# Optimization experiments

Measured on AMD Instinct MI355X. Metric: run time of the kernel, lower is better.

The kernel has to match this reference:

```python
import jax, jax.numpy as jnp
import numpy as np

DIM = 128
HOP = 2
NEIGH = [12, 2]  # neighbor_num per hop
ALPHA = 0.2      # leaky-relu slope
NUM_NODE = 50000
B, S = 128, 50
STDV = 1.0 / np.sqrt(DIM)


def _leaky(x):
    return jnp.where(x >= 0, x, ALPHA * x)


def _local_agg(h, adj, a_local):
    # h: [B,S,D], adj: [B,S,S] ints in 0..4, a_local: [4,D]
    a_in = h[:, :, None, :] * h[:, None, :, :]            # [B,S,S,D]
    e = _leaky(jnp.einsum('bijd,kd->kbij', a_in, a_local))  # [4,B,S,S]
    att = jnp.full(adj.shape, -9e15, dtype=h.dtype)
    for k in range(4):
        att = jnp.where(adj == k + 1, e[k], att)
    att = jax.nn.softmax(att, axis=-1)
    return jnp.einsum('bij,bjd->bid', att, h)


def _global_agg(self_v, neigh_v, extra_v, w1, w2, w3, bias):
    # self_v: [B,N,D], neigh_v: [B,N,K,D], extra_v: [B,N,D]
    a = _leaky(jnp.einsum('bnkd,de->bnke', extra_v[:, :, None, :] * neigh_v, w1))
    a = jnp.einsum('bnke,e->bnk', a, w2)
    a = jax.nn.softmax(a, axis=-1)
    agg = jnp.einsum('bnk,bnkd->bnd', a, neigh_v)
    out = jnp.concatenate([self_v, agg], axis=-1) @ w3 + bias
    return jax.nn.relu(out)


def setup_inputs() -> dict:
    key = jax.random.key(0)
    ks = jax.random.split(key, 12)
    u = lambda k, shp: jax.random.uniform(k, shp, jnp.float32, -STDV, STDV)
    return {
        'inputs': jax.random.randint(ks[0], (B, S), 0, NUM_NODE),
        'adj': jax.random.randint(ks[1], (B, S, S), 0, 5),
        'mask_item': jnp.ones((B, S), dtype=jnp.int32),
        'item': jax.random.randint(ks[2], (B, S), 0, NUM_NODE),
        'first_adj': jax.random.randint(ks[3], (B, S * NEIGH[0]), 0, NUM_NODE),
        'adj_all': jax.random.randint(ks[4], (NUM_NODE, 2), 0, NUM_NODE),
        'embedding': u(ks[5], (NUM_NODE, DIM)),
        'a_local': u(ks[6], (4, DIM)),
        'gw1': u(ks[7], (HOP, DIM, DIM)),
        'gw2': u(ks[8], (HOP, DIM)),
        'gw3': u(ks[9], (HOP, 2 * DIM, DIM)),
        'gbias': u(ks[10], (HOP, DIM)),
    }


def reference(inputs, adj, mask_item, item, first_adj, adj_all,
              embedding, a_local, gw1, gw2, gw3, gbias):
    b, s = inputs.shape
    h = embedding[inputs]                                  # [B,S,D]
    h_local = _local_agg(h, adj, a_local)

    m = mask_item.astype(embedding.dtype)[..., None]       # [B,S,1]
    item_emb = embedding[item] * m
    sum_item = jnp.sum(item_emb, 1) / jnp.sum(m, 1)        # [B,D]
    sess = sum_item[:, None, :]                            # [B,1,D]

    # multi-hop neighbor sampling
    neigh1 = first_adj.reshape(b, s * NEIGH[0])            # [B, 600]
    neigh2 = adj_all[neigh1.reshape(-1)].reshape(b, s * NEIGH[0] * NEIGH[1])  # [B,1200]
    ev = [embedding[inputs], embedding[neigh1], embedding[neigh2]]

    for n_hop in range(HOP):
        nxt = []
        for hop in range(HOP - n_hop):
            neigh_v = ev[hop + 1].reshape(b, -1, NEIGH[hop], DIM)
            extra_v = jnp.broadcast_to(sess, (b, ev[hop].shape[1], DIM))
            nxt.append(_global_agg(ev[hop], neigh_v, extra_v,
                                   gw1[n_hop], gw2[n_hop], gw3[n_hop], gbias[n_hop]))
        ev = nxt
    h_global = ev[0].reshape(b, s, DIM)

    # dropout is identity at eval
    return h_local + h_global
```

## Files before the change

### kernel.cpp

```cpp
#include <hip/hip_runtime.h>
#include <stdint.h>

typedef unsigned short ushort_t;
typedef __attribute__((ext_vector_type(8))) short bf16x8;
typedef __attribute__((ext_vector_type(4))) float f32x4;

#define B_   128
#define S_   50
#define D_   128
#define ALPHA_ 0.2f

__device__ __forceinline__ float bf2f(ushort_t u){
  return __uint_as_float(((uint32_t)u) << 16);
}
__device__ __forceinline__ ushort_t f2bf(float f){
  uint32_t x = __float_as_uint(f);
  x = (x + 0x7fffu + ((x >> 16) & 1u)) >> 16;
  return (ushort_t)x;
}
__device__ __forceinline__ float leaky(float x){ return x >= 0.f ? x : ALPHA_*x; }

__device__ __forceinline__ int detect_flag_block(const uint32_t* __restrict__ emb_raw){
  __shared__ int flg;
  if (threadIdx.x == 0){
    int ok = 1;
    for (int i = 0; i < 64; i++){
      uint32_t lo = emb_raw[i] & 0xffffu;
      uint32_t ex = (lo >> 7) & 0xFFu;
      if (!(lo == 0u || (ex >= 64u && ex <= 126u))) ok = 0;
    }
    flg = ok;
  }
  __syncthreads();
  return flg;
}

#define NLOCAL_ 512
#define NSESS_  64
#define NCVT_   3174
#define NPREP_  48
#define CVT_BASE_   (NLOCAL_ + NSESS_)
#define PREP_BASE_  (CVT_BASE_ + NCVT_)
#define K1_GRID_    (PREP_BASE_ + NPREP_)

__global__ __launch_bounds__(256) void k1(
    const int* __restrict__ inputs, const int* __restrict__ adj,
    const int* __restrict__ item, const int* __restrict__ mask,
    const void* __restrict__ p0, const void* __restrict__ p1,
    const void* __restrict__ p2, const void* __restrict__ p3,
    const void* __restrict__ p4, const void* __restrict__ p5,
    ushort_t* __restrict__ emb_b, uint4* __restrict__ w1f, uint4* __restrict__ w3f,
    ushort_t* __restrict__ sessb, ushort_t* __restrict__ hlb)
{
  int blk = blockIdx.x, tid = threadIdx.x;
  int flag = detect_flag_block((const uint32_t*)p0);

  if (blk < NLOCAL_){
    __shared__ ushort_t hS[64][136];
    __shared__ float    attS[16][68];
    __shared__ int      sids[64];
    __shared__ ushort_t alS[512];
    int b  = blk >> 2;
    int mi = blk & 3;
    if (tid < 64) sids[tid] = (tid < S_) ? inputs[b*S_ + tid] : 0;
    for (int i = tid; i < 512; i += 256)
      alS[i] = flag ? ((const ushort_t*)p1)[i] : f2bf(((const float*)p1)[i]);
    __syncthreads();
    if (flag){
      const ushort_t* e16 = (const ushort_t*)p0;
      for (int idx = tid; idx < 64*16; idx += 256){
        int j = idx >> 4, ch = idx & 15;
        uint4 v = {0u, 0u, 0u, 0u};
        if (j < S_) v = *(const uint4*)(e16 + (size_t)sids[j]*D_ + ch*8);
        *(uint4*)(&hS[j][ch*8]) = v;
      }
    } else {
      const float* ef = (const float*)p0;
      for (int idx = tid; idx < 64*32; idx += 256){
        int j = idx >> 5, ch = idx & 31;
        union { ushort_t u[4]; uint2 d2; } o;
        o.d2 = make_uint2(0u, 0u);
        if (j < S_){
          float4 v = *(const float4*)(ef + (size_t)sids[j]*D_ + ch*4);
          o.u[0]=f2bf(v.x); o.u[1]=f2bf(v.y); o.u[2]=f2bf(v.z); o.u[3]=f2bf(v.w);
        }
        *(uint2*)(&hS[j][ch*4]) = o.d2;
      }
    }
    for (int idx = tid; idx < 16*64; idx += 256)
      attS[idx >> 6][idx & 63] = -9.0e15f;
    __syncthreads();

    int lane = tid & 63, wv = tid >> 6;
    int q = lane >> 4, c = lane & 15;

    f32x4 Eacc[4];
    #pragma unroll
    for (int ni = 0; ni < 4; ni++) Eacc[ni] = (f32x4){0.f,0.f,0.f,0.f};
    #pragma unroll
    for (int kt = 0; kt < 4; kt++){
      uint4 av = *(const uint4*)(alS + wv*D_ + kt*32 + q*8);
      const uint32_t* ap = (const uint32_t*)&av;
      uint4 hv = *(const uint4*)(&hS[mi*16 + c][kt*32 + q*8]);
      const uint32_t* hp = (const uint32_t*)&hv;
      union { ushort_t u[8]; bf16x8 v; } afr;
      #pragma unroll
      for (int p = 0; p < 4; p++){
        float x0 = __uint_as_float(hp[p] << 16)         * __uint_as_float(ap[p] << 16);
        float x1 = __uint_as_float(hp[p] & 0xffff0000u) * __uint_as_float(ap[p] & 0xffff0000u);
        afr.u[2*p]   = f2bf(x0);
        afr.u[2*p+1] = f2bf(x1);
      }
      #pragma unroll
      for (int ni = 0; ni < 4; ni++){
        union { uint4 q4; bf16x8 v; } bfr;
        bfr.q4 = *(const uint4*)(&hS[ni*16 + c][kt*32 + q*8]);
        Eacc[ni] = __builtin_amdgcn_mfma_f32_16x16x32_bf16(afr.v, bfr.v, Eacc[ni], 0,0,0);
      }
    }
    const int* adjb = adj + (size_t)b*S_*S_;
    #pragma unroll
    for (int ni = 0; ni < 4; ni++){
      int j = ni*16 + c;
      #pragma unroll
      for (int r = 0; r < 4; r++){
        int i = mi*16 + q*4 + r;
        if (i < S_ && j < S_){
          int kk = adjb[i*S_ + j];
          if (kk == wv + 1) attS[q*4 + r][j] = leaky(Eacc[ni][r]);
        }
      }
    }
    __syncthreads();
    {
      int r  = tid >> 4;
      int cg = tid & 15;
      int i  = mi*16 + r;
      float v0 = attS[r][cg*4+0], v1 = attS[r][cg*4+1];
      float v2 = attS[r][cg*4+2], v3 = attS[r][cg*4+3];
      float mx = fmaxf(fmaxf(v0,v1), fmaxf(v2,v3));
      #pragma unroll
      for (int off = 1; off < 16; off <<= 1) mx = fmaxf(mx, __shfl_xor(mx, off, 16));
      float e0 = (cg*4+0 < S_) ? __expf(v0 - mx) : 0.f;
      float e1 = (cg*4+1 < S_) ? __expf(v1 - mx) : 0.f;
      float e2 = (cg*4+2 < S_) ? __expf(v2 - mx) : 0.f;
      float e3 = (cg*4+3 < S_) ? __expf(v3 - mx) : 0.f;
      float s = e0 + e1 + e2 + e3;
      #pragma unroll
      for (int off = 1; off < 16; off <<= 1) s += __shfl_xor(s, off, 16);
      float inv = (i < S_) ? 1.f / s : 0.f;
      attS[r][cg*4+0] = e0*inv;
      attS[r][cg*4+1] = e1*inv;
      attS[r][cg*4+2] = e2*inv;
      attS[r][cg*4+3] = e3*inv;
    }
    __syncthreads();
    f32x4 Pacc[2];
    Pacc[0] = (f32x4){0.f,0.f,0.f,0.f};
    Pacc[1] = (f32x4){0.f,0.f,0.f,0.f};
    #pragma unroll
    for (int kt = 0; kt < 2; kt++){
      union { ushort_t u[8]; bf16x8 v; } afr;
      const float* arow = &attS[c][kt*32 + q*8];
      #pragma unroll
      for (int j = 0; j < 8; j++) afr.u[j] = f2bf(arow[j]);
      #pragma unroll
      for (int nn = 0; nn < 2; nn++){
        int ni = 2*wv + nn;
        union { ushort_t u[8]; bf16x8 v; } bfr;
        #pragma unroll
        for (int jj = 0; jj < 8; jj++)
          bfr.u[jj] = hS[kt*32 + q*8 + jj][ni*16 + c];
        Pacc[nn] = __builtin_amdgcn_mfma_f32_16x16x32_bf16(afr.v, bfr.v, Pacc[nn], 0,0,0);
      }
    }
    #pragma unroll
    for (int nn = 0; nn < 2; nn++){
      int d = (2*wv + nn)*16 + c;
      #pragma unroll
      for (int r = 0; r < 4; r++){
        int i = mi*16 + q*4 + r;
        if (i < S_) hlb[((size_t)b*S_ + i)*D_ + d] = f2bf(Pacc[nn][r]);
      }
    }
  } else if (blk < CVT_BASE_){
    int b = (blk - NLOCAL_)*2 + (tid >> 7);
    int d = tid & 127;
    float acc = 0.f, den = 0.f;
    if (flag){
      const ushort_t* e16 = (const ushort_t*)p0;
      for (int s = 0; s < S_; s++){
        float fm = (float)mask[b*S_ + s];
        int id = item[b*S_ + s];
        acc += fm * bf2f(e16[(size_t)id*D_ + d]);
        den += fm;
      }
    } else {
      const float* ef = (const float*)p0;
      for (int s = 0; s < S_; s++){
        float fm = (float)mask[b*S_ + s];
        int id = item[b*S_ + s];
        acc += fm * ef[(size_t)id*D_ + d];
        den += fm;
      }
    }
    sessb[b*D_ + d] = f2bf(acc / den);
  } else if (blk < PREP_BASE_){
    const int seg_end[6] = {6400000, 6400512, 6433280, 6433536, 6499072, 6499328};
    int base = ((blk - CVT_BASE_)*256 + tid) * 8;
    if (base >= 6499328) return;
    int s = 0;
    while (base >= seg_end[s]) s++;
    int segbase = (s == 0) ? 0 : seg_end[s-1];
    const void* src = (s==0)?p0:(s==1)?p1:(s==2)?p2:(s==3)?p3:(s==4)?p4:p5;
    int off = base - segbase;
    union { ushort_t u[8]; uint4 q4; } o;
    if (flag){
      o.q4 = *(const uint4*)((const ushort_t*)src + off);
    } else {
      const float* fp = (const float*)src + off;
      float4 v0 = *(const float4*)(fp);
      float4 v1 = *(const float4*)(fp + 4);
      o.u[0]=f2bf(v0.x); o.u[1]=f2bf(v0.y); o.u[2]=f2bf(v0.z); o.u[3]=f2bf(v0.w);
      o.u[4]=f2bf(v1.x); o.u[5]=f2bf(v1.y); o.u[6]=f2bf(v1.z); o.u[7]=f2bf(v1.w);
    }
    *(uint4*)(emb_b + base) = o.q4;
  } else {
    int id = (blk - PREP_BASE_)*256 + tid;
    if (id >= 12288) return;
    if (id < 4096){
      int h = id >> 11, i = id & 2047;
      int kt = i >> 9, rem = i & 511, t = rem >> 6, ln = rem & 63;
      int q = ln >> 4, c = ln & 15;
      union { ushort_t u[8]; uint4 q4; } e;
      #pragma unroll
      for (int j = 0; j < 8; j++){
        int idx = h*16384 + (32*kt + q*8 + j)*128 + 16*t + c;
        e.u[j] = flag ? ((const ushort_t*)p2)[idx] : f2bf(((const float*)p2)[idx]);
      }
      w1f[h*2048 + i] = e.q4;
    } else {
      int id2 = id - 4096;
      int h = id2 >> 12, i = id2 & 4095;
      int kt = i >> 9, rem = i & 511, t = rem >> 6, ln = rem & 63;
      int q = ln >> 4, c = ln & 15;
      union { ushort_t u[8]; uint4 q4; } e;
      #pragma unroll
      for (int j = 0; j < 8; j++){
        int idx = h*32768 + (32*kt + q*8 + j)*128 + 16*t + c;
        e.u[j] = flag ? ((const ushort_t*)p4)[idx] : f2bf(((const float*)p4)[idx]);
      }
      w3f[h*4096 + i] = e.q4;
    }
  }
}

#define NT2TPREP_ 1564
#define NT2SCORE_ 768
#define K2_GRID_  (NT2TPREP_ + NT2SCORE_)

__global__ __launch_bounds__(256) void k2(
    const ushort_t* __restrict__ emb, const uint4* __restrict__ w3f,
    ushort_t* __restrict__ Tt, ushort_t* __restrict__ Tb,
    const ushort_t* __restrict__ sessb,
    const int* __restrict__ neigh1, const int* __restrict__ adj_all,
    const uint4* __restrict__ w1f, const ushort_t* __restrict__ w2,
    float* __restrict__ score)
{
  __shared__ uint4 frag[2048];
  __shared__ ushort_t sS[128];
  int blk = blockIdx.x, tid = threadIdx.x;

  if (blk < NT2TPREP_){
    int half = blk & 1;
    int rowbase = (blk >> 1) * 64;
    for (int i = tid; i < 2048; i += 256) frag[i] = w3f[half*2048 + i];
    __syncthreads();
    int lane = tid & 63, wave = tid >> 6;
    int m = lane & 15, q = lane >> 4;
    int row = rowbase + wave*16 + m;
    int rowc = row < 50000 ? row : 49999;
    f32x4 acc[8];
    #pragma unroll
    for (int t = 0; t < 8; t++) acc[t] = (f32x4){0.f,0.f,0.f,0.f};
    #pragma unroll
    for (int kt = 0; kt < 4; kt++){
      union { uint4 q4; bf16x8 v; } bfr;
      bfr.q4 = *(const uint4*)(emb + (size_t)rowc*D_ + kt*32 + q*8);
      #pragma unroll
      for (int t = 0; t < 8; t++){
        union { uint4 q4; bf16x8 v; } af;
        af.q4 = frag[(kt*8 + t)*64 + lane];
        acc[t] = __builtin_amdgcn_mfma_f32_16x16x32_bf16(af.v, bfr.v, acc[t], 0, 0, 0);
      }
    }
    if (row < 50000){
      ushort_t* dst = (half ? Tb : Tt) + (size_t)row*D_;
      #pragma unroll
      for (int t = 0; t < 8; t++){
        int col0 = 16*t + q*4;
        union { ushort_t u[4]; uint2 d2; } pk;
        #pragma unroll
        for (int r = 0; r < 4; r++) pk.u[r] = f2bf(acc[t][r]);
        *(uint2*)(dst + col0) = pk.d2;
      }
    }
    return;
  }

  int b2  = blk - NT2TPREP_;
  int sb  = b2 / 6;
  int sub = b2 - sb*6;
  int grp = sub >> 1;
  int halft = sub & 1;
  if (tid < 16) ((uint4*)sS)[tid] = ((const uint4*)(sessb + (size_t)sb*D_))[tid];
  __syncthreads();
  for (int i = tid; i < 2048; i += 256){
    int kt = i >> 9, ln = i & 63, q = (ln >> 4);
    uint4 w = w1f[i];
    uint4 sv = *(const uint4*)(sS + kt*32 + q*8);
    const ushort_t* wu = (const ushort_t*)&w;
    const ushort_t* su = (const ushort_t*)&sv;
    union { ushort_t u[8]; uint4 q4; } o;
    #pragma unroll
    for (int j = 0; j < 8; j++) o.u[j] = f2bf(bf2f(wu[j]) * bf2f(su[j]));
    frag[i] = o.q4;
  }
  __syncthreads();
  int lane = tid & 63, wave = tid >> 6;
  int m = lane & 15, q = lane >> 4;
  float w2v[8];
  #pragma unroll
  for (int t = 0; t < 8; t++) w2v[t] = bf2f(w2[16*t + m]);

  int tend = halft ? 38 : 19;
  for (int t = halft*19 + wave; t < tend; t += 4){
    int rr = t*16 + m;
    int rrc = rr < 599 ? rr : 599;
    int nid;
    if (grp == 0){
      nid = neigh1[sb*600 + rrc];
    } else {
      int r2 = sb*1200 + (grp-1)*600 + rrc;
      nid = adj_all[(size_t)neigh1[r2 >> 1]*2 + (r2 & 1)];
    }
    const ushort_t* nrow = emb + (size_t)nid*D_;
    f32x4 acc[8];
    #pragma unroll
    for (int t8 = 0; t8 < 8; t8++) acc[t8] = (f32x4){0.f,0.f,0.f,0.f};
    #pragma unroll
    for (int kt = 0; kt < 4; kt++){
      union { uint4 q4; bf16x8 v; } af;
      af.q4 = *(const uint4*)(nrow + kt*32 + q*8);
      #pragma unroll
      for (int t8 = 0; t8 < 8; t8++){
        union { uint4 q4; bf16x8 v; } bf;
        bf.q4 = frag[(kt*8 + t8)*64 + lane];
        acc[t8] = __builtin_amdgcn_mfma_f32_16x16x32_bf16(af.v, bf.v, acc[t8], 0, 0, 0);
      }
    }
    #pragma unroll
    for (int r = 0; r < 4; r++){
      float s = 0.f;
      #pragma unroll
      for (int t8 = 0; t8 < 8; t8++) s += leaky(acc[t8][r]) * w2v[t8];
      s += __shfl_xor(s, 1, 64);
      s += __shfl_xor(s, 2, 64);
      s += __shfl_xor(s, 4, 64);
      s += __shfl_xor(s, 8, 64);
      if (m == 0){
        int rw = t*16 + q*4 + r;
        if (rw < 600){
          int sidx = (grp == 0) ? (sb*600 + rw)
                                : (76800 + sb*1200 + (grp-1)*600 + rw);
          score[sidx] = s;
        }
      }
    }
  }
}

__global__ __launch_bounds__(256) void score2_c(
    const ushort_t* __restrict__ sessb, const ushort_t* __restrict__ out1,
    const uint4* __restrict__ w1f, const ushort_t* __restrict__ w2,
    float* __restrict__ score)
{
  __shared__ uint4 bfrag[2048];
  __shared__ ushort_t sS[128];
  int blk = blockIdx.x, tid = threadIdx.x;
  int sb  = blk >> 2;
  int qtr = blk & 3;
  if (tid < 16) ((uint4*)sS)[tid] = ((const uint4*)(sessb + (size_t)sb*D_))[tid];
  __syncthreads();
  for (int i = tid; i < 2048; i += 256){
    int kt = i >> 9, ln = i & 63, q = (ln >> 4);
    uint4 w = w1f[i];
    uint4 sv = *(const uint4*)(sS + kt*32 + q*8);
    const ushort_t* wu = (const ushort_t*)&w;
    const ushort_t* su = (const ushort_t*)&sv;
    union { ushort_t u[8]; uint4 q4; } o;
    #pragma unroll
    for (int j = 0; j < 8; j++) o.u[j] = f2bf(bf2f(wu[j]) * bf2f(su[j]));
    bfrag[i] = o.q4;
  }
  __syncthreads();
  int lane = tid & 63, wave = tid >> 6;
  int m = lane & 15, q = lane >> 4;
  float w2v[8];
  #pragma unroll
  for (int t = 0; t < 8; t++) w2v[t] = bf2f(w2[16*t + m]);

  int t0 = qtr*10, tend = (qtr*10 + 10 < 38) ? qtr*10 + 10 : 38;
  for (int t = t0 + wave; t < tend; t += 4){
    int rr = t*16 + m;
    int rrc = rr < 599 ? rr : 599;
    const ushort_t* nrow = out1 + ((size_t)sb*600 + rrc)*D_;
    f32x4 acc[8];
    #pragma unroll
    for (int t8 = 0; t8 < 8; t8++) acc[t8] = (f32x4){0.f,0.f,0.f,0.f};
    #pragma unroll
    for (int kt = 0; kt < 4; kt++){
      union { uint4 q4; bf16x8 v; } af;
      af.q4 = *(const uint4*)(nrow + kt*32 + q*8);
      #pragma unroll
      for (int t8 = 0; t8 < 8; t8++){
        union { uint4 q4; bf16x8 v; } bf;
        bf.q4 = bfrag[(kt*8 + t8)*64 + lane];
        acc[t8] = __builtin_amdgcn_mfma_f32_16x16x32_bf16(af.v, bf.v, acc[t8], 0, 0, 0);
      }
    }
    #pragma unroll
    for (int r = 0; r < 4; r++){
      float s = 0.f;
      #pragma unroll
      for (int t8 = 0; t8 < 8; t8++) s += leaky(acc[t8][r]) * w2v[t8];
      s += __shfl_xor(s, 1, 64);
      s += __shfl_xor(s, 2, 64);
      s += __shfl_xor(s, 4, 64);
      s += __shfl_xor(s, 8, 64);
      if (m == 0){
        int rw = t*16 + q*4 + r;
        if (rw < 600) score[sb*600 + rw] = s;
      }
    }
  }
}

template<int K>
__device__ __forceinline__ void softmaxK(const float* __restrict__ sc, float att[K]){
  float mx = -__builtin_inff();
  #pragma unroll
  for (int k = 0; k < K; k++){ att[k] = sc[k]; mx = fmaxf(mx, att[k]); }
  float s = 0.f;
  #pragma unroll
  for (int k = 0; k < K; k++){ att[k] = __expf(att[k] - mx); s += att[k]; }
  float inv = 1.f / s;
  #pragma unroll
  for (int k = 0; k < K; k++) att[k] *= inv;
}

template<int K>
__device__ __forceinline__ void out_tile(
    int lane, const uint4* __restrict__ afrag,
    const ushort_t* __restrict__ sptr, const ushort_t* const nptr[K],
    const float att[K], f32x4 acc[8]){
  int q = lane >> 4;
  #pragma unroll
  for (int kt = 0; kt < 8; kt++){
    union { ushort_t u[8]; uint4 q4; bf16x8 v; } bfr;
    if (kt < 4){
      bfr.q4 = *(const uint4*)(sptr + kt*32 + q*8);
    } else {
      float g[8] = {0,0,0,0,0,0,0,0};
      #pragma unroll
      for (int k = 0; k < K; k++){
        uint4 nv = *(const uint4*)(nptr[k] + (kt-4)*32 + q*8);
        const uint32_t* np = (const uint32_t*)&nv;
        #pragma unroll
        for (int p = 0; p < 4; p++){
          g[2*p]   = fmaf(att[k], __uint_as_float(np[p] << 16),         g[2*p]);
          g[2*p+1] = fmaf(att[k], __uint_as_float(np[p] & 0xffff0000u), g[2*p+1]);
        }
      }
      #pragma unroll
      for (int j = 0; j < 8; j++) bfr.u[j] = f2bf(g[j]);
    }
    #pragma unroll
    for (int t = 0; t < 8; t++){
      union { uint4 q4; bf16x8 v; } af;
      af.q4 = afrag[(kt*8 + t)*64 + lane];
      acc[t] = __builtin_amdgcn_mfma_f32_16x16x32_bf16(af.v, bfr.v, acc[t], 0, 0, 0);
    }
  }
}

__global__ __launch_bounds__(256) void gather_out(
    const int* __restrict__ idx, const int* __restrict__ nbr,
    const int* __restrict__ adj_all, const float* __restrict__ score,
    const ushort_t* __restrict__ Tt, const ushort_t* __restrict__ Tb,
    const ushort_t* __restrict__ bias,
    ushort_t* __restrict__ o0c, ushort_t* __restrict__ out1c,
    int nA50, int nTot, int scoreBbase)
{
  int row  = (blockIdx.x*256 + threadIdx.x) >> 6;
  int lane = threadIdx.x & 63;
  if (row >= nTot) return;
  row = __builtin_amdgcn_readfirstlane(row);
  float b0 = bf2f(bias[lane*2]), b1 = bf2f(bias[lane*2 + 1]);
  float acc0, acc1;
  ushort_t* dst;
  if (row < nA50){
    float att[12];
    softmaxK<12>(score + (size_t)row*12, att);
    uint32_t sv = *(const uint32_t*)(Tt + (size_t)idx[row]*D_ + lane*2);
    acc0 = __uint_as_float(sv << 16);
    acc1 = __uint_as_float(sv & 0xffff0000u);
    #pragma unroll
    for (int k = 0; k < 12; k++){
      uint32_t nv = *(const uint32_t*)(Tb + (size_t)nbr[row*12 + k]*D_ + lane*2);
      acc0 = fmaf(att[k], __uint_as_float(nv << 16),          acc0);
      acc1 = fmaf(att[k], __uint_as_float(nv & 0xffff0000u),  acc1);
    }
    dst = o0c + (size_t)row*D_;
  } else {
    int rB = row - nA50;
    float att[2];
    softmaxK<2>(score + scoreBbase + (size_t)rB*2, att);
    int self = nbr[rB];
    uint32_t sv = *(const uint32_t*)(Tt + (size_t)self*D_ + lane*2);
    acc0 = __uint_as_float(sv << 16);
    acc1 = __uint_as_float(sv & 0xffff0000u);
    #pragma unroll
    for (int k = 0; k < 2; k++){
      uint32_t nv = *(const uint32_t*)(Tb + (size_t)adj_all[(size_t)self*2 + k]*D_ + lane*2);
      acc0 = fmaf(att[k], __uint_as_float(nv << 16),          acc0);
      acc1 = fmaf(att[k], __uint_as_float(nv & 0xffff0000u),  acc1);
    }
    dst = out1c + (size_t)rB*D_;
  }
  union { ushort_t u[2]; uint32_t d; } pk;
  pk.u[0] = f2bf(fmaxf(acc0 + b0, 0.f));
  pk.u[1] = f2bf(fmaxf(acc1 + b1, 0.f));
  *(uint32_t*)(dst + lane*2) = pk.d;
}

__global__ __launch_bounds__(256) void out_mfma_c2(
    const float* __restrict__ score, const ushort_t* __restrict__ out1,
    const ushort_t* __restrict__ selfsrc, const uint4* __restrict__ w3f,
    const ushort_t* __restrict__ bias,
    const ushort_t* __restrict__ addsrc, float* __restrict__ outf, int nrows){
  __shared__ uint4 afrag[4096];
  int tid = threadIdx.x;
  for (int i = tid; i < 4096; i += 256) afrag[i] = w3f[i];
  __syncthreads();
  int lane = tid & 63, wave = tid >> 6;
  int mrow = lane & 15, q = lane >> 4;
  float bv[8][4];
  #pragma unroll
  for (int t = 0; t < 8; t++){
    const ushort_t* bp = bias + 16*t + q*4;
    #pragma unroll
    for (int r = 0; r < 4; r++) bv[t][r] = bf2f(bp[r]);
  }
  int row_base = blockIdx.x*64 + wave*16;
  int row = row_base + mrow;
  bool active = row < nrows;
  int rowc = active ? row : (nrows - 1);
  const ushort_t* sptr = selfsrc + (size_t)rowc*D_;
  const ushort_t* nptr[12];
  #pragma unroll
  for (int k = 0; k < 12; k++) nptr[k] = out1 + (size_t)(rowc*12 + k)*D_;
  float att[12];
  softmaxK<12>(score + (size_t)rowc*12, att);
  f32x4 acc[8];
  #pragma unroll
  for (int t = 0; t < 8; t++) acc[t] = (f32x4){0.f,0.f,0.f,0.f};
  out_tile<12>(lane, afrag, sptr, nptr, att, acc);
  if (active){
    #pragma unroll
    for (int t = 0; t < 8; t++){
      int col0 = 16*t + q*4;
      float v[4];
      const ushort_t* ap = addsrc + (size_t)row*D_ + col0;
      #pragma unroll
      for (int r = 0; r < 4; r++)
        v[r] = fmaxf(acc[t][r] + bv[t][r], 0.f) + bf2f(ap[r]);
      *(f32x4*)(outf + (size_t)row*D_ + col0) = (f32x4){v[0], v[1], v[2], v[3]};
    }
  }
}

__global__ __launch_bounds__(256) void score_mfma_ab(
    const ushort_t* __restrict__ sessb, const ushort_t* __restrict__ emb,
    const int* __restrict__ neigh1, const int* __restrict__ adj_all,
    const uint4* __restrict__ w1f, const ushort_t* __restrict__ w2,
    float* __restrict__ score, int nA){
  __shared__ uint4 bfrag[2048];
  int tid = threadIdx.x;
  for (int i = tid; i < 2048; i += 256) bfrag[i] = w1f[i];
  __syncthreads();
  int lane = tid & 63, wave = tid >> 6;
  int m = lane & 15, q = lane >> 4;
  float w2v[8];
  #pragma unroll
  for (int t = 0; t < 8; t++) w2v[t] = bf2f(w2[16*t + m]);

  for (int it = 0; it < 2; it++){
    int row_base = blockIdx.x*128 + it*64 + wave*16;
    int row = row_base + m;
    const ushort_t* nrow; int b;
    if (row < nA){
      nrow = emb + (size_t)neigh1[row]*D_;
      b = row / 600;
    } else {
      int r2 = row - nA;
      nrow = emb + (size_t)adj_all[(size_t)neigh1[r2>>1]*2 + (r2&1)]*D_;
      b = r2 / 1200;
    }
    const ushort_t* srow = sessb + (size_t)b*D_;

    f32x4 acc[8];
    #pragma unroll
    for (int t = 0; t < 8; t++) acc[t] = (f32x4){0.f,0.f,0.f,0.f};
    #pragma unroll
    for (int kt = 0; kt < 4; kt++){
      uint4 nv = *(const uint4*)(nrow + kt*32 + q*8);
      uint4 sv = *(const uint4*)(srow + kt*32 + q*8);
      const uint32_t* np = (const uint32_t*)&nv;
      const uint32_t* sp = (const uint32_t*)&sv;
      union { ushort_t u[8]; bf16x8 v; } afr;
      #pragma unroll
      for (int p = 0; p < 4; p++){
        uint32_t n2 = np[p], s2 = sp[p];
        float a0 = __uint_as_float(n2 << 16)          * __uint_as_float(s2 << 16);
        float a1 = __uint_as_float(n2 & 0xffff0000u)  * __uint_as_float(s2 & 0xffff0000u);
        afr.u[2*p]   = f2bf(a0);
        afr.u[2*p+1] = f2bf(a1);
      }
      #pragma unroll
      for (int t = 0; t < 8; t++){
        union { uint4 q4; bf16x8 v; } bfr;
        bfr.q4 = bfrag[(kt*8 + t)*64 + lane];
        acc[t] = __builtin_amdgcn_mfma_f32_16x16x32_bf16(afr.v, bfr.v, acc[t], 0, 0, 0);
      }
    }
    #pragma unroll
    for (int r = 0; r < 4; r++){
      float s = 0.f;
      #pragma unroll
      for (int t = 0; t < 8; t++) s += leaky(acc[t][r]) * w2v[t];
      s += __shfl_xor(s, 1, 64);
      s += __shfl_xor(s, 2, 64);
      s += __shfl_xor(s, 4, 64);
      s += __shfl_xor(s, 8, 64);
      if (m == 0) score[row_base + q*4 + r] = s;
    }
  }
}

__global__ __launch_bounds__(256) void score_mfma_c(
    const ushort_t* __restrict__ sessb, const ushort_t* __restrict__ out1,
    const uint4* __restrict__ w1f, const ushort_t* __restrict__ w2,
    float* __restrict__ score){
  __shared__ uint4 bfrag[2048];
  int tid = threadIdx.x;
  for (int i = tid; i < 2048; i += 256) bfrag[i] = w1f[i];
  __syncthreads();
  int lane = tid & 63, wave = tid >> 6;
  int m = lane & 15, q = lane >> 4;
  float w2v[8];
  #pragma unroll
  for (int t = 0; t < 8; t++) w2v[t] = bf2f(w2[16*t + m]);
  for (int it = 0; it < 2; it++){
    int row_base = blockIdx.x*128 + it*64 + wave*16;
    int row = row_base + m;
    const ushort_t* nrow = out1 + (size_t)row*D_;
    int b = row / 600;
    const ushort_t* srow = sessb + (size_t)b*D_;
    f32x4 acc[8];
    #pragma unroll
    for (int t = 0; t < 8; t++) acc[t] = (f32x4){0.f,0.f,0.f,0.f};
    #pragma unroll
    for (int kt = 0; kt < 4; kt++){
      uint4 nv = *(const uint4*)(nrow + kt*32 + q*8);
      uint4 sv = *(const uint4*)(srow + kt*32 + q*8);
      const uint32_t* np = (const uint32_t*)&nv;
      const uint32_t* sp = (const uint32_t*)&sv;
      union { ushort_t u[8]; bf16x8 v; } afr;
      #pragma unroll
      for (int p = 0; p < 4; p++){
        uint32_t n2 = np[p], s2 = sp[p];
        float a0 = __uint_as_float(n2 << 16)          * __uint_as_float(s2 << 16);
        float a1 = __uint_as_float(n2 & 0xffff0000u)  * __uint_as_float(s2 & 0xffff0000u);
        afr.u[2*p]   = f2bf(a0);
        afr.u[2*p+1] = f2bf(a1);
      }
      #pragma unroll
      for (int t = 0; t < 8; t++){
        union { uint4 q4; bf16x8 v; } bfr;
        bfr.q4 = bfrag[(kt*8 + t)*64 + lane];
        acc[t] = __builtin_amdgcn_mfma_f32_16x16x32_bf16(afr.v, bfr.v, acc[t], 0, 0, 0);
      }
    }
    #pragma unroll
    for (int r = 0; r < 4; r++){
      float s = 0.f;
      #pragma unroll
      for (int t = 0; t < 8; t++) s += leaky(acc[t][r]) * w2v[t];
      s += __shfl_xor(s, 1, 64);
      s += __shfl_xor(s, 2, 64);
      s += __shfl_xor(s, 4, 64);
      s += __shfl_xor(s, 8, 64);
      if (m == 0) score[row_base + q*4 + r] = s;
    }
  }
}

__global__ __launch_bounds__(512) void out_mfma_ab(
    const float* __restrict__ score, const int* __restrict__ idx,
    const int* __restrict__ nbr, const int* __restrict__ adj_all,
    const ushort_t* __restrict__ emb, const uint4* __restrict__ w3f,
    const ushort_t* __restrict__ bias,
    ushort_t* __restrict__ o0c, ushort_t* __restrict__ out1c,
    int nA, int nTot, int scoreBbase){
  __shared__ uint4 afrag[4096];
  int tid = threadIdx.x;
  for (int i = tid; i < 4096; i += 512) afrag[i] = w3f[i];
  __syncthreads();
  int lane = tid & 63, wave = tid >> 6;
  int mrow = lane & 15, q = lane >> 4;
  float bv[8][4];
  #pragma unroll
  for (int t = 0; t < 8; t++){
    const ushort_t* bp = bias + 16*t + q*4;
    #pragma unroll
    for (int r = 0; r < 4; r++) bv[t][r] = bf2f(bp[r]);
  }
  int row_base = blockIdx.x*128 + wave*16;
  int row = row_base + mrow;
  bool active = row < nTot;
  int rowc = active ? row : (nTot - 1);
  bool isA = rowc < nA;
  f32x4 acc[8];
  #pragma unroll
  for (int t = 0; t < 8; t++) acc[t] = (f32x4){0.f,0.f,0.f,0.f};
  if (isA){
    const ushort_t* sptr = emb + (size_t)idx[rowc]*D_;
    const ushort_t* nptr[12];
    #pragma unroll
    for (int k = 0; k < 12; k++) nptr[k] = emb + (size_t)nbr[rowc*12 + k]*D_;
    float att[12];
    softmaxK<12>(score + (size_t)rowc*12, att);
    out_tile<12>(lane, afrag, sptr, nptr, att, acc);
  } else {
    int rB = rowc - nA;
    const ushort_t* sptr = emb + (size_t)nbr[rB]*D_;
    const ushort_t* nptr[2];
    #pragma unroll
    for (int k = 0; k < 2; k++) nptr[k] = emb + (size_t)adj_all[(size_t)nbr[rB]*2 + k]*D_;
    float att[2];
    softmaxK<2>(score + scoreBbase + (size_t)rB*2, att);
    out_tile<2>(lane, afrag, sptr, nptr, att, acc);
  }
  if (active){
    ushort_t* dst = isA ? (o0c + (size_t)row*D_) : (out1c + (size_t)(row - nA)*D_);
    #pragma unroll
    for (int t = 0; t < 8; t++){
      int col0 = 16*t + q*4;
      union { ushort_t u[4]; uint2 d2; } pk;
      #pragma unroll
      for (int r = 0; r < 4; r++) pk.u[r] = f2bf(fmaxf(acc[t][r] + bv[t][r], 0.f));
      *(uint2*)(dst + col0) = pk.d2;
    }
  }
}

__global__ __launch_bounds__(512) void out_mfma_c(
    const float* __restrict__ score, const ushort_t* __restrict__ out1,
    const ushort_t* __restrict__ selfsrc, const uint4* __restrict__ w3f,
    const ushort_t* __restrict__ bias,
    const ushort_t* __restrict__ addsrc, float* __restrict__ outf, int nrows){
  __shared__ uint4 afrag[4096];
  int tid = threadIdx.x;
  for (int i = tid; i < 4096; i += 512) afrag[i] = w3f[i];
  __syncthreads();
  int lane = tid & 63, wave = tid >> 6;
  int mrow = lane & 15, q = lane >> 4;
  float bv[8][4];
  #pragma unroll
  for (int t = 0; t < 8; t++){
    const ushort_t* bp = bias + 16*t + q*4;
    #pragma unroll
    for (int r = 0; r < 4; r++) bv[t][r] = bf2f(bp[r]);
  }
  int row_base = blockIdx.x*128 + wave*16;
  int row = row_base + mrow;
  bool active = row < nrows;
  int rowc = active ? row : (nrows - 1);
  const ushort_t* sptr = selfsrc + (size_t)rowc*D_;
  const ushort_t* nptr[12];
  #pragma unroll
  for (int k = 0; k < 12; k++) nptr[k] = out1 + (size_t)(rowc*12 + k)*D_;
  float att[12];
  softmaxK<12>(score + (size_t)rowc*12, att);
  f32x4 acc[8];
  #pragma unroll
  for (int t = 0; t < 8; t++) acc[t] = (f32x4){0.f,0.f,0.f,0.f};
  out_tile<12>(lane, afrag, sptr, nptr, att, acc);
  if (active){
    #pragma unroll
    for (int t = 0; t < 8; t++){
      int col0 = 16*t + q*4;
      float v[4];
      const ushort_t* ap = addsrc + (size_t)row*D_ + col0;
      #pragma unroll
      for (int r = 0; r < 4; r++)
        v[r] = fmaxf(acc[t][r] + bv[t][r], 0.f) + bf2f(ap[r]);
      *(f32x4*)(outf + (size_t)row*D_ + col0) = (f32x4){v[0], v[1], v[2], v[3]};
    }
  }
}

extern "C" void kernel_launch(void* const* d_in, const int* in_sizes, int n_in,
                              void* d_out, int out_size, void* d_ws, size_t ws_size,
                              hipStream_t stream) {
  const int* inputs    = (const int*)d_in[0];
  const int* adj       = (const int*)d_in[1];
  const int* mask_item = (const int*)d_in[2];
  const int* item      = (const int*)d_in[3];
  const int* first_adj = (const int*)d_in[4];
  const int* adj_all   = (const int*)d_in[5];

  char* ws = (char*)d_ws;
  size_t o = 0;
  ushort_t* emb_b  = (ushort_t*)(ws + o); o += 12800000;
  ushort_t* alocb  = (ushort_t*)(ws + o); o += 1024;
  ushort_t* gw1b   = (ushort_t*)(ws + o); o += 65536;
  ushort_t* gw2b   = (ushort_t*)(ws + o); o += 512;
  ushort_t* gw3b   = (ushort_t*)(ws + o); o += 131072;
  ushort_t* gbb    = (ushort_t*)(ws + o); o += 512;
  ushort_t* sessb  = (ushort_t*)(ws + o); o += 32768;
  ushort_t* hlb    = (ushort_t*)(ws + o); o += 1638400;
  uint4*    w1f    = (uint4*)(ws + o);    o += 65536;
  uint4*    w3f    = (uint4*)(ws + o);    o += 131072;
  size_t fixed = o;
  (void)alocb; (void)gw1b; (void)gw3b;

  float* outp = (float*)d_out;

  const size_t TPATH_NEED = fixed + 2*(size_t)12800000
                          + (size_t)128*153600
                          + (size_t)128*12800
                          + (size_t)3*128*600*4;
  bool tpath = (ws_size >= TPATH_NEED);

  k1<<<K1_GRID_, 256, 0, stream>>>(
      inputs, adj, item, mask_item,
      d_in[6], d_in[7], d_in[8], d_in[9], d_in[10], d_in[11],
      emb_b, w1f, w3f, sessb, hlb);

  if (tpath){
    ushort_t* Tt    = (ushort_t*)(ws + o);  o += 12800000;
    ushort_t* Tb    = (ushort_t*)(ws + o);  o += 12800000;
    ushort_t* out1c = (ushort_t*)(ws + o);  o += (size_t)128*153600;
    ushort_t* o0c   = (ushort_t*)(ws + o);  o += (size_t)128*12800;
    float*    score = (float*)(ws + o);
    int nA600 = 128*600, nA50 = 128*50, nTot = 128*650;

    k2<<<K2_GRID_, 256, 0, stream>>>(emb_b, w3f, Tt, Tb,
                                     sessb, first_adj, adj_all,
                                     w1f, gw2b, score);
    gather_out<<<(nTot*64 + 255)/256, 256, 0, stream>>>(inputs, first_adj, adj_all, score,
                                                        Tt, Tb, gbb, o0c, out1c,
                                                        nA50, nTot, nA600);
    score2_c<<<512, 256, 0, stream>>>(sessb, out1c, w1f + 2048, gw2b + 128, score);
    out_mfma_c2<<<(nA50 + 63)/64, 256, 0, stream>>>(score, out1c, o0c,
                                                    w3f + 4096, gbb + 128,
                                                    hlb, outp, nA50);
  } else {
    int CHB = 16;
    if      (ws_size >= fixed + (size_t)128*173600) CHB = 128;
    else if (ws_size >= fixed + (size_t)64 *173600) CHB = 64;
    else if (ws_size >= fixed + (size_t)32 *173600) CHB = 32;
    ushort_t* out1c = (ushort_t*)(ws + o);  o += (size_t)CHB*153600;
    ushort_t* o0c   = (ushort_t*)(ws + o);  o += (size_t)CHB*12800;
    float*    score = (float*)(ws + o);

    int nchunk = B_ / CHB;
    for (int c = 0; c < nchunk; c++){
      int b0 = c * CHB;
      const int* fadj  = first_adj + (size_t)b0 * 600;
      const ushort_t* sbc = sessb + (size_t)b0 * D_;
      ushort_t*  hlc   = hlb  + (size_t)b0 * 50 * D_;
      float*     outc  = outp + (size_t)b0 * 50 * D_;
      int nA600 = CHB*600, nA50 = CHB*50, nTot = CHB*650;

      score_mfma_ab<<<(3*nA600)/128, 256, 0, stream>>>(sbc, emb_b, fadj, adj_all,
                                                       w1f, gw2b, score, nA600);
      out_mfma_ab<<<(nTot + 127)/128, 512, 0, stream>>>(score, inputs + b0*50, fadj, adj_all,
                                                        emb_b, w3f, gbb, o0c, out1c,
                                                        nA50, nTot, nA600);
      score_mfma_c<<<nA600/128, 256, 0, stream>>>(sbc, out1c, w1f + 2048, gw2b + 128, score);
      out_mfma_c<<<(nA50 + 127)/128, 512, 0, stream>>>(score, out1c, o0c,
                                                       w3f + 4096, gbb + 128,
                                                       hlc, outc, nA50);
    }
  }
}
```

Before: 195.4 us.

## Skip bf16 embedding copy when input is bf16; reorder and coarsen T-prep blocks

When the embedding table is already bf16 and the T-precompute path is used, k1 no longer copies the whole table into a workspace buffer, and k2 reads the original input directly. The T-prep blocks in k2 now each handle four 64-row tiles, which cuts the grid from 1564 to 392 prep blocks and reuses the weight fragments loaded into shared memory. Those blocks are also placed after the score blocks in the grid. The aim is to remove a 12.8 MB copy and repeated shared-memory fragment loads. In exchange, each prep block does more serial work, and any later kernel that still reads emb_b would see stale data when the input is bf16.

```diff
diff --git a/kernel.cpp b/kernel.cpp
--- a/kernel.cpp
+++ b/kernel.cpp
@@ -50,7 +50,7 @@
     const void* __restrict__ p2, const void* __restrict__ p3,
     const void* __restrict__ p4, const void* __restrict__ p5,
     ushort_t* __restrict__ emb_b, uint4* __restrict__ w1f, uint4* __restrict__ w3f,
-    ushort_t* __restrict__ sessb, ushort_t* __restrict__ hlb)
+    ushort_t* __restrict__ sessb, ushort_t* __restrict__ hlb, int skip_emb)
 {
   int blk = blockIdx.x, tid = threadIdx.x;
   int flag = detect_flag_block((const uint32_t*)p0);
@@ -209,6 +209,7 @@
     const int seg_end[6] = {6400000, 6400512, 6433280, 6433536, 6499072, 6499328};
     int base = ((blk - CVT_BASE_)*256 + tid) * 8;
     if (base >= 6499328) return;
+    if (flag && skip_emb && base < 6400000) return;
     int s = 0;
     while (base >= seg_end[s]) s++;
     int segbase = (s == 0) ? 0 : seg_end[s-1];
@@ -255,12 +256,13 @@
   }
 }
 
-#define NT2TPREP_ 1564
 #define NT2SCORE_ 768
-#define K2_GRID_  (NT2TPREP_ + NT2SCORE_)
+#define NT2TPREP_ 392
+#define K2_GRID_  (NT2SCORE_ + NT2TPREP_)
 
 __global__ __launch_bounds__(256) void k2(
-    const ushort_t* __restrict__ emb, const uint4* __restrict__ w3f,
+    const void* __restrict__ p0, const ushort_t* __restrict__ emb_b,
+    const uint4* __restrict__ w3f,
     ushort_t* __restrict__ Tt, ushort_t* __restrict__ Tb,
     const ushort_t* __restrict__ sessb,
     const int* __restrict__ neigh1, const int* __restrict__ adj_all,
@@ -270,45 +272,52 @@
   __shared__ uint4 frag[2048];
   __shared__ ushort_t sS[128];
   int blk = blockIdx.x, tid = threadIdx.x;
-
-  if (blk < NT2TPREP_){
-    int half = blk & 1;
-    int rowbase = (blk >> 1) * 64;
+  int flag = detect_flag_block((const uint32_t*)p0);
+  const ushort_t* emb = flag ? (const ushort_t*)p0 : emb_b;
+
+  if (blk >= NT2SCORE_){
+    int tp   = blk - NT2SCORE_;
+    int half = tp & 1;
+    int rowbase0 = (tp >> 1) * 256;
     for (int i = tid; i < 2048; i += 256) frag[i] = w3f[half*2048 + i];
     __syncthreads();
     int lane = tid & 63, wave = tid >> 6;
     int m = lane & 15, q = lane >> 4;
-    int row = rowbase + wave*16 + m;
-    int rowc = row < 50000 ? row : 49999;
-    f32x4 acc[8];
-    #pragma unroll
-    for (int t = 0; t < 8; t++) acc[t] = (f32x4){0.f,0.f,0.f,0.f};
-    #pragma unroll
-    for (int kt = 0; kt < 4; kt++){
-      union { uint4 q4; bf16x8 v; } bfr;
-      bfr.q4 = *(const uint4*)(emb + (size_t)rowc*D_ + kt*32 + q*8);
-      #pragma unroll
-      for (int t = 0; t < 8; t++){
-        union { uint4 q4; bf16x8 v; } af;
-        af.q4 = frag[(kt*8 + t)*64 + lane];
-        acc[t] = __builtin_amdgcn_mfma_f32_16x16x32_bf16(af.v, bfr.v, acc[t], 0, 0, 0);
-      }
-    }
-    if (row < 50000){
-      ushort_t* dst = (half ? Tb : Tt) + (size_t)row*D_;
-      #pragma unroll
-      for (int t = 0; t < 8; t++){
-        int col0 = 16*t + q*4;
-        union { ushort_t u[4]; uint2 d2; } pk;
+    ushort_t* Tdst = half ? Tb : Tt;
+    #pragma unroll
+    for (int rit = 0; rit < 4; rit++){
+      int row = rowbase0 + rit*64 + wave*16 + m;
+      int rowc = row < 50000 ? row : 49999;
+      f32x4 acc[8];
+      #pragma unroll
+      for (int t = 0; t < 8; t++) acc[t] = (f32x4){0.f,0.f,0.f,0.f};
+      #pragma unroll
+      for (int kt = 0; kt < 4; kt++){
+        union { uint4 q4; bf16x8 v; } bfr;
+        bfr.q4 = *(const uint4*)(emb + (size_t)rowc*D_ + kt*32 + q*8);
         #pragma unroll
-        for (int r = 0; r < 4; r++) pk.u[r] = f2bf(acc[t][r]);
-        *(uint2*)(dst + col0) = pk.d2;
+        for (int t = 0; t < 8; t++){
+          union { uint4 q4; bf16x8 v; } af;
+          af.q4 = frag[(kt*8 + t)*64 + lane];
+          acc[t] = __builtin_amdgcn_mfma_f32_16x16x32_bf16(af.v, bfr.v, acc[t], 0, 0, 0);
+        }
+      }
+      if (row < 50000){
+        ushort_t* dst = Tdst + (size_t)row*D_;
+        #pragma unroll
+        for (int t = 0; t < 8; t++){
+          int col0 = 16*t + q*4;
+          union { ushort_t u[4]; uint2 d2; } pk;
+          #pragma unroll
+          for (int r = 0; r < 4; r++) pk.u[r] = f2bf(acc[t][r]);
+          *(uint2*)(dst + col0) = pk.d2;
+        }
       }
     }
     return;
   }
 
-  int b2  = blk - NT2TPREP_;
+  int b2  = blk;
   int sb  = b2 / 6;
   int sub = b2 - sb*6;
   int grp = sub >> 1;
@@ -857,7 +866,7 @@
   k1<<<K1_GRID_, 256, 0, stream>>>(
       inputs, adj, item, mask_item,
       d_in[6], d_in[7], d_in[8], d_in[9], d_in[10], d_in[11],
-      emb_b, w1f, w3f, sessb, hlb);
+      emb_b, w1f, w3f, sessb, hlb, tpath ? 1 : 0);
 
   if (tpath){
     ushort_t* Tt    = (ushort_t*)(ws + o);  o += 12800000;
@@ -867,7 +876,7 @@
     float*    score = (float*)(ws + o);
     int nA600 = 128*600, nA50 = 128*50, nTot = 128*650;
 
-    k2<<<K2_GRID_, 256, 0, stream>>>(emb_b, w3f, Tt, Tb,
+    k2<<<K2_GRID_, 256, 0, stream>>>(d_in[6], emb_b, w3f, Tt, Tb,
                                      sessb, first_adj, adj_all,
                                      w1f, gw2b, score);
     gather_out<<<(nTot*64 + 255)/256, 256, 0, stream>>>(inputs, first_adj, adj_all, score,
```

Result: faster. 187.6 us (-4.0%).
